# Optimization experiments

Hardware: AMD Instinct MI355X
Metric: run time of the kernel (lower is better)

## Reference

```python
import jax, jax.numpy as jnp
import numpy as np
import math

N_HEAD = 8
FACTOR = 1


def setup_inputs() -> dict:
    key = jax.random.key(0)
    kq, kk, kv = jax.random.split(key, 3)
    B, L, D = 16, 2048, 512
    return {
        "queries": jax.random.normal(kq, (B, L, D), dtype=jnp.float32),
        "keys": jax.random.normal(kk, (B, L, D), dtype=jnp.float32),
        "values": jax.random.normal(kv, (B, L, D), dtype=jnp.float32),
    }


def _autocorrelation(queries, keys, values):
    B, L, D = queries.shape
    H = N_HEAD
    E = D // H
    top_k = int(FACTOR * math.log(L))  # static: L is a Python int

    # (B,L,H,E) -> (B,H,E,L)
    q = queries.reshape(B, L, H, E).transpose(0, 2, 3, 1)
    k = keys.reshape(B, L, H, E).transpose(0, 2, 3, 1)
    v = values.reshape(B, L, H, E).transpose(0, 2, 3, 1)

    # period-based dependencies via FFT cross-correlation
    qf = jnp.fft.rfft(q, axis=-1)
    kf = jnp.fft.rfft(k, axis=-1)
    corr = jnp.fft.irfft(qf * jnp.conj(kf), n=L, axis=-1)  # (B,H,E,L)

    # time-delay aggregation (training path)
    mean_value = corr.mean(axis=(1, 2))                      # (B,L)
    index = jax.lax.top_k(mean_value.mean(axis=0), top_k)[1]  # (top_k,)
    weights = mean_value[:, index]                            # (B,top_k)
    tmp_corr = jax.nn.softmax(weights, axis=-1)               # (B,top_k)

    # roll values by each top-k delay and combine with softmax weights
    patterns = jax.vmap(lambda d: jnp.roll(v, -d, axis=-1))(index)  # (k,B,H,E,L)
    V = jnp.einsum('kbhel,bk->bhel', patterns, tmp_corr)            # (B,H,E,L)

    out = V.transpose(0, 3, 1, 2).reshape(B, L, D)
    corr_out = corr.transpose(0, 3, 1, 2).reshape(B, L, D)
    return out, corr_out


def reference(queries, keys, values):
    return _autocorrelation(queries, keys, values)
```

## Files before the change

kernel.cpp:

```cpp
#include <hip/hip_runtime.h>
#include <math.h>

#define B_  16
#define L_  2048
#define D_  512
#define K_  7
#define Q_  (B_*L_*D_)

__device__ __forceinline__ ushort f2bf(float x){
  uint u = __float_as_uint(x);
  u += 0x7FFFu + ((u >> 16) & 1u);
  return (ushort)(u >> 16);
}
__device__ __forceinline__ float bf2f(ushort h){
  return __uint_as_float((uint)h << 16);
}

__global__ __launch_bounds__(256) void kA(const float* __restrict__ q,
                                          const float* __restrict__ k,
                                          ushort* __restrict__ qT,
                                          ushort* __restrict__ kT) {
  __shared__ float t[64][65];
  const int l0 = blockIdx.x * 64, d0 = blockIdx.y * 64;
  const int b = blockIdx.z & 15, ten = blockIdx.z >> 4;
  const float*  __restrict__ src = ten ? k : q;
  ushort* __restrict__ dst = ten ? kT : qT;
  const int tid = threadIdx.x;
  const size_t ibase = (size_t)b * L_ * D_;
#pragma unroll
  for (int u = 0; u < 4; ++u) {
    const int idx = tid + (u << 8);
    const int row = idx >> 4;
    const int c   = (idx & 15) << 2;
    const float4 v = *(const float4*)&src[ibase + (size_t)(l0 + row) * D_ + d0 + c];
    t[row][c + 0] = v.x; t[row][c + 1] = v.y;
    t[row][c + 2] = v.z; t[row][c + 3] = v.w;
  }
  __syncthreads();
  const size_t obase = (size_t)b * D_ * L_;
#pragma unroll
  for (int u = 0; u < 4; ++u) {
    const int idx  = tid + (u << 8);
    const int drow = idx >> 4;
    const int c    = (idx & 15) << 2;
    ushort4 o;
    o.x = f2bf(t[c + 0][drow]); o.y = f2bf(t[c + 1][drow]);
    o.z = f2bf(t[c + 2][drow]); o.w = f2bf(t[c + 3][drow]);
    *(ushort4*)&dst[obase + (size_t)(d0 + drow) * L_ + l0 + c] = o;
  }
}

struct cf { float r, i; };
__device__ __forceinline__ cf cadd(cf a, cf b){ return {a.r+b.r, a.i+b.i}; }
__device__ __forceinline__ cf csub(cf a, cf b){ return {a.r-b.r, a.i-b.i}; }
__device__ __forceinline__ cf cmul(cf a, cf b){ return {a.r*b.r - a.i*b.i, a.r*b.i + a.i*b.r}; }
template<bool INV> __device__ __forceinline__ cf rot90(cf x){
  return INV ? cf{-x.i, x.r} : cf{x.i, -x.r};
}
__device__ __forceinline__ int swz(int a){ return a ^ (((a >> 4) ^ (a >> 8)) & 15); }
__device__ __forceinline__ cf ldx(const float2* __restrict__ p, int i){
  const float2 v = p[swz(i)]; return {v.x, v.y};
}
__device__ __forceinline__ void stx(float2* __restrict__ p, int i, cf v){
  p[swz(i)] = {v.r, v.i};
}

template<bool INV>
__device__ __forceinline__ void dft8(cf a[8], cf b[8]) {
  const float H = 0.70710678118654752440f;
  cf t0 = cadd(a[0],a[4]), t1 = cadd(a[1],a[5]), t2 = cadd(a[2],a[6]), t3 = cadd(a[3],a[7]);
  cf u0 = csub(a[0],a[4]), u1 = csub(a[1],a[5]), u2 = csub(a[2],a[6]), u3 = csub(a[3],a[7]);
  const cf w1 = INV ? cf{H,  H} : cf{ H, -H};
  const cf w3 = INV ? cf{-H, H} : cf{-H, -H};
  u1 = cmul(u1, w1);
  u2 = rot90<INV>(u2);
  u3 = cmul(u3, w3);
  { cf s0 = cadd(t0,t2), s1 = csub(t0,t2), s2 = cadd(t1,t3), s3 = rot90<INV>(csub(t1,t3));
    b[0]=cadd(s0,s2); b[4]=csub(s0,s2); b[2]=cadd(s1,s3); b[6]=csub(s1,s3); }
  { cf s0 = cadd(u0,u2), s1 = csub(u0,u2), s2 = cadd(u1,u3), s3 = rot90<INV>(csub(u1,u3));
    b[1]=cadd(s0,s2); b[5]=csub(s0,s2); b[3]=cadd(s1,s3); b[7]=csub(s1,s3); }
}

template<int LOG2S>
__device__ __forceinline__ void twiddle_store(cf b[8], float2* __restrict__ dst,
                                              int j, int p, float sgn_ang) {
  float sn, cs;
  __sincosf(sgn_ang * (float)(p << LOG2S), &sn, &cs);
  const cf w1{cs, sn};
  const cf w2 = cmul(w1, w1);
  const cf w3 = cmul(w2, w1);
  const cf w4 = cmul(w2, w2);
  const cf w5 = cmul(w3, w2);
  const cf w6 = cmul(w3, w3);
  const cf w7 = cmul(w4, w3);
  b[1] = cmul(b[1], w1); b[2] = cmul(b[2], w2); b[3] = cmul(b[3], w3);
  b[4] = cmul(b[4], w4); b[5] = cmul(b[5], w5); b[6] = cmul(b[6], w6);
  b[7] = cmul(b[7], w7);
  const int wb = j + 7 * (p << LOG2S);
#pragma unroll
  for (int k = 0; k < 8; ++k) stx(dst, wb + (k << LOG2S), b[k]);
}

#define ANG_ (-0.0030679615757712823f)

__device__ __forceinline__ void pass8_first(const ushort* __restrict__ qg,
                                            const ushort* __restrict__ kg,
                                            float2* __restrict__ dst, int j) {
  cf a[8], b[8];
#pragma unroll
  for (int l = 0; l < 8; ++l) {
    const int ix = j + (l << 8);
    a[l] = {bf2f(qg[ix]), bf2f(kg[ix])};
  }
  dft8<false>(a, b);
  twiddle_store<0>(b, dst, j, j, ANG_);
}

template<int LOG2S, bool INV>
__device__ __forceinline__ void pass8f2(const float2* __restrict__ src,
                                        float2* __restrict__ dst, int j) {
  const int p = j >> LOG2S;
  cf a[8], b[8];
#pragma unroll
  for (int l = 0; l < 8; ++l) a[l] = ldx(src, j + (l << 8));
  dft8<INV>(a, b);
  twiddle_store<LOG2S>(b, dst, j, p, INV ? -ANG_ : ANG_);
}

__device__ __forceinline__ void pass4_fwd(const float2* __restrict__ src,
                                          float2* __restrict__ dst, int j) {
#pragma unroll
  for (int h = 0; h < 2; ++h) {
    const int jj = j + (h << 8);
    cf a0 = ldx(src, jj), a1 = ldx(src, jj + 512), a2 = ldx(src, jj + 1024), a3 = ldx(src, jj + 1536);
    cf s0 = cadd(a0,a2), s1 = csub(a0,a2), s2 = cadd(a1,a3), s3 = rot90<false>(csub(a1,a3));
    stx(dst, jj,        cadd(s0,s2));
    stx(dst, jj + 512,  cadd(s1,s3));
    stx(dst, jj + 1024, csub(s0,s2));
    stx(dst, jj + 1536, csub(s1,s3));
  }
}

__device__ __forceinline__ void pass4_last(const float2* __restrict__ src,
                                           ushort* __restrict__ c0,
                                           ushort* __restrict__ c1, int j) {
  const float inv = 1.0f / (float)L_;
#pragma unroll
  for (int h = 0; h < 2; ++h) {
    const int jj = j + (h << 8);
    cf a0 = ldx(src, jj), a1 = ldx(src, jj + 512), a2 = ldx(src, jj + 1024), a3 = ldx(src, jj + 1536);
    cf s0 = cadd(a0,a2), s1 = csub(a0,a2), s2 = cadd(a1,a3), s3 = rot90<true>(csub(a1,a3));
    const cf o0 = cadd(s0,s2), o1 = cadd(s1,s3), o2 = csub(s0,s2), o3 = csub(s1,s3);
    c0[jj]        = f2bf(o0.r * inv);  c1[jj]        = f2bf(o0.i * inv);
    c0[jj + 512]  = f2bf(o1.r * inv);  c1[jj + 512]  = f2bf(o1.i * inv);
    c0[jj + 1024] = f2bf(o2.r * inv);  c1[jj + 1024] = f2bf(o2.i * inv);
    c0[jj + 1536] = f2bf(o3.r * inv);  c1[jj + 1536] = f2bf(o3.i * inv);
  }
}

__global__ __launch_bounds__(256) void kB(const ushort* __restrict__ qT,
                                          const ushort* __restrict__ kT,
                                          ushort* __restrict__ corrT) {
  __shared__ float2 A[L_];
  __shared__ float2 Bb[L_];
  const int tid = threadIdx.x;
  const size_t row0 = (size_t)(blockIdx.x * 2) * L_;
  const size_t row1 = row0 + L_;

  pass8_first(qT + row0, kT + row0, Bb, tid); __syncthreads();
  pass8f2<3, false>(Bb, A, tid);              __syncthreads();
  pass8f2<6, false>(A, Bb, tid);              __syncthreads();
  pass4_fwd(Bb, A, tid);                      __syncthreads();

  float s1r[4], s1i[4];
#pragma unroll
  for (int u = 0; u < 4; ++u) {
    const int f = tid + (u << 8);
    if (f == 0) {
      const cf z0 = ldx(A, 0), zn = ldx(A, 1024);
      s1r[u] = z0.r * z0.i;
      s1i[u] = zn.r * zn.i;
    } else {
      const cf a = ldx(A, f), am = ldx(A, 2048 - f);
      const float qr = 0.5f * (a.r + am.r), qi = 0.5f * (a.i - am.i);
      const float kr = 0.5f * (a.i + am.i), ki = 0.5f * (am.r - a.r);
      s1r[u] = qr * kr + qi * ki;
      s1i[u] = qi * kr - qr * ki;
    }
  }

  pass8_first(qT + row1, kT + row1, Bb, tid); __syncthreads();
  pass8f2<3, false>(Bb, A, tid);              __syncthreads();
  pass8f2<6, false>(A, Bb, tid);              __syncthreads();
  pass4_fwd(Bb, A, tid);                      __syncthreads();

#pragma unroll
  for (int u = 0; u < 4; ++u) {
    const int f = tid + (u << 8);
    if (f == 0) {
      const cf z0 = ldx(A, 0), zn = ldx(A, 1024);
      const float s2_0 = z0.r * z0.i, s2_n = zn.r * zn.i;
      stx(Bb, 0,    {s1r[0], s2_0});
      stx(Bb, 1024, {s1i[0], s2_n});
    } else {
      const cf a = ldx(A, f), am = ldx(A, 2048 - f);
      const float qr = 0.5f * (a.r + am.r), qi = 0.5f * (a.i - am.i);
      const float kr = 0.5f * (a.i + am.i), ki = 0.5f * (am.r - a.r);
      const float s2r = qr * kr + qi * ki, s2i = qi * kr - qr * ki;
      stx(Bb, f,        {s1r[u] - s2i,  s1i[u] + s2r});
      stx(Bb, 2048 - f, {s1r[u] + s2i, -s1i[u] + s2r});
    }
  }
  __syncthreads();

  pass8f2<0, true>(Bb, A, tid);               __syncthreads();
  pass8f2<3, true>(A, Bb, tid);               __syncthreads();
  pass8f2<6, true>(Bb, A, tid);               __syncthreads();
  pass4_last(A, corrT + row0, corrT + row1, tid);
}

__global__ __launch_bounds__(256) void kC(const ushort* __restrict__ corrT,
                                          float* __restrict__ corrOut,
                                          float* __restrict__ partial) {
  __shared__ float t[64][65];
  const int t0 = blockIdx.x * 64, d0 = blockIdx.y * 64, b = blockIdx.z;
  const int tid = threadIdx.x;
#pragma unroll
  for (int u = 0; u < 4; ++u) {
    const int idx  = tid + (u << 8);
    const int drow = idx >> 4;
    const int c    = (idx & 15) << 2;
    const ushort4 v = *(const ushort4*)&corrT[((size_t)b * D_ + d0 + drow) * L_ + t0 + c];
    t[drow][c + 0] = bf2f(v.x); t[drow][c + 1] = bf2f(v.y);
    t[drow][c + 2] = bf2f(v.z); t[drow][c + 3] = bf2f(v.w);
  }
  __syncthreads();
#pragma unroll
  for (int u = 0; u < 4; ++u) {
    const int idx  = tid + (u << 8);
    const int trow = idx >> 4;
    const int c    = (idx & 15) << 2;
    float4 o;
    o.x = t[c + 0][trow]; o.y = t[c + 1][trow];
    o.z = t[c + 2][trow]; o.w = t[c + 3][trow];
    *(float4*)&corrOut[((size_t)b * L_ + t0 + trow) * D_ + d0 + c] = o;
  }
  if (tid < 64) {
    float s = 0.f;
#pragma unroll
    for (int i = 0; i < 64; ++i) s += t[i][tid];
    partial[((size_t)b * 8 + blockIdx.y) * L_ + t0 + tid] = s;
  }
}

__global__ __launch_bounds__(256) void kD0(const float* __restrict__ partial,
                                           float* __restrict__ g) {
  __shared__ float red[4][64];
  const int tl = threadIdx.x & 63, rg = threadIdx.x >> 6;
  const int tau = blockIdx.x * 64 + tl;
  float s = 0.f;
  for (int i = rg; i < 128; i += 4) s += partial[(size_t)i * L_ + tau];
  red[rg][tl] = s;
  __syncthreads();
  if (rg == 0) g[tau] = red[0][tl] + red[1][tl] + red[2][tl] + red[3][tl];
}

__global__ __launch_bounds__(256) void kD1(const float* __restrict__ gin,
                                           const float* __restrict__ partial,
                                           int* __restrict__ oidx,
                                           float* __restrict__ ow) {
  __shared__ float g[L_];
  __shared__ float rv[256];
  __shared__ int   ri[256];
  __shared__ int   sidx[K_];
  const int tid = threadIdx.x;
#pragma unroll
  for (int u = 0; u < 8; ++u) g[tid + u * 256] = gin[tid + u * 256];
  __syncthreads();

  for (int it = 0; it < K_; ++it) {
    float bv = -1e30f; int bix = 1 << 30;
#pragma unroll
    for (int u = 0; u < 8; ++u) {
      const int tau = tid + u * 256;
      const float vv = g[tau];
      if (vv > bv || (vv == bv && tau < bix)) { bv = vv; bix = tau; }
    }
    rv[tid] = bv; ri[tid] = bix;
    __syncthreads();
    for (int off = 128; off > 0; off >>= 1) {
      if (tid < off) {
        const float v2 = rv[tid + off]; const int i2 = ri[tid + off];
        if (v2 > rv[tid] || (v2 == rv[tid] && i2 < ri[tid])) {
          rv[tid] = v2; ri[tid] = i2;
        }
      }
      __syncthreads();
    }
    if (tid == 0) { sidx[it] = ri[0]; g[ri[0]] = -3e38f; }
    __syncthreads();
  }

  if (tid < B_) {
    const int b = tid;
    float m[K_]; float mx = -1e30f;
    for (int kk = 0; kk < K_; ++kk) {
      float s = 0.f;
      for (int dt = 0; dt < 8; ++dt)
        s += partial[((size_t)b * 8 + dt) * L_ + sidx[kk]];
      m[kk] = s * (1.0f / 512.0f);
      mx = fmaxf(mx, m[kk]);
    }
    float sum = 0.f;
    for (int kk = 0; kk < K_; ++kk) { m[kk] = expf(m[kk] - mx); sum += m[kk]; }
    const float inv = 1.0f / sum;
    for (int kk = 0; kk < K_; ++kk) ow[b * K_ + kk] = m[kk] * inv;
  }
  if (tid < K_) oidx[tid] = sidx[tid];
}

__global__ __launch_bounds__(256) void kE(const float4* __restrict__ v4,
                                          const float* __restrict__ w,
                                          const int* __restrict__ idx,
                                          float4* __restrict__ out4) {
  const int bx = blockIdx.x;
  const int b  = bx >> 10;
  const int l  = ((bx & 1023) << 1) | (threadIdx.x >> 7);
  const int j  = threadIdx.x & 127;

  float ww[K_]; int rr[K_];
#pragma unroll
  for (int kk = 0; kk < K_; ++kk) {
    ww[kk] = w[b * K_ + kk];
    int r = l + idx[kk];
    if (r >= L_) r -= L_;
    rr[kk] = r;
  }
  const size_t vb = (size_t)b * L_ * 128;
  float4 acc = make_float4(0.f, 0.f, 0.f, 0.f);
#pragma unroll
  for (int kk = 0; kk < K_; ++kk) {
    const float4 vv = v4[vb + (size_t)rr[kk] * 128 + j];
    acc.x += ww[kk] * vv.x; acc.y += ww[kk] * vv.y;
    acc.z += ww[kk] * vv.z; acc.w += ww[kk] * vv.w;
  }
  out4[vb + (size_t)l * 128 + j] = acc;
}

extern "C" void kernel_launch(void* const* d_in, const int* in_sizes, int n_in,
                              void* d_out, int out_size, void* d_ws, size_t ws_size,
                              hipStream_t stream) {
  const float* q = (const float*)d_in[0];
  const float* k = (const float*)d_in[1];
  const float* v = (const float*)d_in[2];

  float* out     = (float*)d_out;
  float* corrOut = out + Q_;
  ushort* qT16 = (ushort*)out;
  ushort* kT16 = (ushort*)corrOut;

  ushort* corrT16 = (ushort*)d_ws;
  float*  partial = (float*)(corrT16 + Q_);
  float*  g2048   = partial + (size_t)B_ * 8 * L_;
  int*    oidx    = (int*)(g2048 + L_);
  float*  ow      = (float*)(oidx + 16);

  kA<<<dim3(L_ / 64, D_ / 64, B_ * 2), 256, 0, stream>>>(q, k, qT16, kT16);
  kB<<<(B_ * D_) / 2, 256, 0, stream>>>(qT16, kT16, corrT16);
  kC<<<dim3(L_ / 64, D_ / 64, B_), 256, 0, stream>>>(corrT16, corrOut, partial);
  kD0<<<32, 256, 0, stream>>>(partial, g2048);
  kD1<<<1, 256, 0, stream>>>(g2048, partial, oidx, ow);
  kE<<<(B_ * L_) / 2, 256, 0, stream>>>((const float4*)v, ow, oidx, (float4*)out);
}
```

Baseline: 187.2 us.

## Restructure 2048-point FFT from radix-8/8/8/4 into radix-16/16/8 passes

Replaces the four-pass shared-memory FFT (three radix-8 passes plus a radix-4 pass) with three passes: two radix-16 stages run by half the threads and a final radix-8 stage, for both forward and inverse transforms. This cuts the number of shared-memory round trips and barriers per transform. In exchange, half the block idles during the radix-16 stages, register pressure rises with 16-point butterflies, and the strided shared-memory store pattern may cause bank conflicts.

After: 210.2 us. +12.3%, slower.

```diff
diff --git a/kernel.cpp b/kernel.cpp
--- a/kernel.cpp
+++ b/kernel.cpp
@@ -81,80 +81,117 @@
     b[1]=cadd(s0,s2); b[5]=csub(s0,s2); b[3]=cadd(s1,s3); b[7]=csub(s1,s3); }
 }
 
-template<int LOG2S>
-__device__ __forceinline__ void twiddle_store(cf b[8], float2* __restrict__ dst,
-                                              int j, int p, float sgn_ang) {
-  float sn, cs;
-  __sincosf(sgn_ang * (float)(p << LOG2S), &sn, &cs);
+template<bool INV>
+__device__ __forceinline__ void dft16(cf a[16], cf o[16]) {
+  cf e_in[8], o_in[8], E[8], O[8];
+#pragma unroll
+  for (int i = 0; i < 8; ++i) { e_in[i] = a[2*i]; o_in[i] = a[2*i+1]; }
+  dft8<INV>(e_in, E);
+  dft8<INV>(o_in, O);
+  const float C1 = 0.92387953251128675613f, S1 = 0.38268343236508977173f;
+  const float H  = 0.70710678118654752440f;
+  const float sg = INV ? 1.0f : -1.0f;
+  const cf w1{ C1, sg*S1}, w2{ H, sg*H}, w3{ S1, sg*C1};
+  const cf w5{-S1, sg*C1}, w6{-H, sg*H}, w7{-C1, sg*S1};
+  cf t;
+  t = O[0];             o[0]=cadd(E[0],t); o[8] =csub(E[0],t);
+  t = cmul(O[1], w1);   o[1]=cadd(E[1],t); o[9] =csub(E[1],t);
+  t = cmul(O[2], w2);   o[2]=cadd(E[2],t); o[10]=csub(E[2],t);
+  t = cmul(O[3], w3);   o[3]=cadd(E[3],t); o[11]=csub(E[3],t);
+  t = rot90<INV>(O[4]); o[4]=cadd(E[4],t); o[12]=csub(E[4],t);
+  t = cmul(O[5], w5);   o[5]=cadd(E[5],t); o[13]=csub(E[5],t);
+  t = cmul(O[6], w6);   o[6]=cadd(E[6],t); o[14]=csub(E[6],t);
+  t = cmul(O[7], w7);   o[7]=cadd(E[7],t); o[15]=csub(E[7],t);
+}
+
+#define ANG_ (-0.0030679615757712823f)
+
+__device__ __forceinline__ void twiddle16(cf b[16], float ang) {
+  float sn, cs; __sincosf(ang, &sn, &cs);
   const cf w1{cs, sn};
-  const cf w2 = cmul(w1, w1);
-  const cf w3 = cmul(w2, w1);
-  const cf w4 = cmul(w2, w2);
-  const cf w5 = cmul(w3, w2);
-  const cf w6 = cmul(w3, w3);
-  const cf w7 = cmul(w4, w3);
-  b[1] = cmul(b[1], w1); b[2] = cmul(b[2], w2); b[3] = cmul(b[3], w3);
-  b[4] = cmul(b[4], w4); b[5] = cmul(b[5], w5); b[6] = cmul(b[6], w6);
-  b[7] = cmul(b[7], w7);
-  const int wb = j + 7 * (p << LOG2S);
-#pragma unroll
-  for (int k = 0; k < 8; ++k) stx(dst, wb + (k << LOG2S), b[k]);
-}
-
-#define ANG_ (-0.0030679615757712823f)
-
-__device__ __forceinline__ void pass8_first(const ushort* __restrict__ qg,
-                                            const ushort* __restrict__ kg,
-                                            float2* __restrict__ dst, int j) {
+  const cf w2 = cmul(w1,w1);
+  const cf w3 = cmul(w2,w1);
+  const cf w4 = cmul(w2,w2);
+  const cf w5 = cmul(w3,w2);
+  const cf w6 = cmul(w3,w3);
+  const cf w7 = cmul(w4,w3);
+  const cf w8 = cmul(w4,w4);
+  const cf w9 = cmul(w5,w4);
+  const cf w10= cmul(w5,w5);
+  const cf w11= cmul(w6,w5);
+  const cf w12= cmul(w6,w6);
+  const cf w13= cmul(w7,w6);
+  const cf w14= cmul(w7,w7);
+  const cf w15= cmul(w8,w7);
+  b[1]=cmul(b[1],w1);  b[2]=cmul(b[2],w2);  b[3]=cmul(b[3],w3);
+  b[4]=cmul(b[4],w4);  b[5]=cmul(b[5],w5);  b[6]=cmul(b[6],w6);
+  b[7]=cmul(b[7],w7);  b[8]=cmul(b[8],w8);  b[9]=cmul(b[9],w9);
+  b[10]=cmul(b[10],w10); b[11]=cmul(b[11],w11); b[12]=cmul(b[12],w12);
+  b[13]=cmul(b[13],w13); b[14]=cmul(b[14],w14); b[15]=cmul(b[15],w15);
+}
+
+__device__ __forceinline__ void p16_first(const ushort* __restrict__ qg,
+                                          const ushort* __restrict__ kg,
+                                          float2* __restrict__ dst, int j) {
+  cf a[16], b[16];
+#pragma unroll
+  for (int l = 0; l < 16; ++l) {
+    const int ix = j + (l << 7);
+    a[l] = {bf2f(qg[ix]), bf2f(kg[ix])};
+  }
+  dft16<false>(a, b);
+  twiddle16(b, ANG_ * (float)j);
+#pragma unroll
+  for (int k = 0; k < 16; ++k) stx(dst, (j << 4) + k, b[k]);
+}
+
+__device__ __forceinline__ void p16_s1_inv(const float2* __restrict__ src,
+                                           float2* __restrict__ dst, int j) {
+  cf a[16], b[16];
+#pragma unroll
+  for (int l = 0; l < 16; ++l) a[l] = ldx(src, j + (l << 7));
+  dft16<true>(a, b);
+  twiddle16(b, -ANG_ * (float)j);
+#pragma unroll
+  for (int k = 0; k < 16; ++k) stx(dst, (j << 4) + k, b[k]);
+}
+
+template<bool INV>
+__device__ __forceinline__ void p16_mid(const float2* __restrict__ src,
+                                        float2* __restrict__ dst, int j) {
+  const int p = j >> 4, q = j & 15;
+  cf a[16], b[16];
+#pragma unroll
+  for (int l = 0; l < 16; ++l) a[l] = ldx(src, j + (l << 7));
+  dft16<INV>(a, b);
+  twiddle16(b, (INV ? -ANG_ : ANG_) * (float)(p << 4));
+  const int base = q + (p << 8);
+#pragma unroll
+  for (int k = 0; k < 16; ++k) stx(dst, base + (k << 4), b[k]);
+}
+
+__device__ __forceinline__ void p8_final(const float2* __restrict__ src,
+                                         float2* __restrict__ dst, int j) {
   cf a[8], b[8];
 #pragma unroll
-  for (int l = 0; l < 8; ++l) {
-    const int ix = j + (l << 8);
-    a[l] = {bf2f(qg[ix]), bf2f(kg[ix])};
-  }
+  for (int l = 0; l < 8; ++l) a[l] = ldx(src, j + (l << 8));
   dft8<false>(a, b);
-  twiddle_store<0>(b, dst, j, j, ANG_);
-}
-
-template<int LOG2S, bool INV>
-__device__ __forceinline__ void pass8f2(const float2* __restrict__ src,
-                                        float2* __restrict__ dst, int j) {
-  const int p = j >> LOG2S;
+#pragma unroll
+  for (int k = 0; k < 8; ++k) stx(dst, j + (k << 8), b[k]);
+}
+
+__device__ __forceinline__ void p8_final_store(const float2* __restrict__ src,
+                                               ushort* __restrict__ c0,
+                                               ushort* __restrict__ c1, int j) {
   cf a[8], b[8];
 #pragma unroll
   for (int l = 0; l < 8; ++l) a[l] = ldx(src, j + (l << 8));
-  dft8<INV>(a, b);
-  twiddle_store<LOG2S>(b, dst, j, p, INV ? -ANG_ : ANG_);
-}
-
-__device__ __forceinline__ void pass4_fwd(const float2* __restrict__ src,
-                                          float2* __restrict__ dst, int j) {
-#pragma unroll
-  for (int h = 0; h < 2; ++h) {
-    const int jj = j + (h << 8);
-    cf a0 = ldx(src, jj), a1 = ldx(src, jj + 512), a2 = ldx(src, jj + 1024), a3 = ldx(src, jj + 1536);
-    cf s0 = cadd(a0,a2), s1 = csub(a0,a2), s2 = cadd(a1,a3), s3 = rot90<false>(csub(a1,a3));
-    stx(dst, jj,        cadd(s0,s2));
-    stx(dst, jj + 512,  cadd(s1,s3));
-    stx(dst, jj + 1024, csub(s0,s2));
-    stx(dst, jj + 1536, csub(s1,s3));
-  }
-}
-
-__device__ __forceinline__ void pass4_last(const float2* __restrict__ src,
-                                           ushort* __restrict__ c0,
-                                           ushort* __restrict__ c1, int j) {
+  dft8<true>(a, b);
   const float inv = 1.0f / (float)L_;
 #pragma unroll
-  for (int h = 0; h < 2; ++h) {
-    const int jj = j + (h << 8);
-    cf a0 = ldx(src, jj), a1 = ldx(src, jj + 512), a2 = ldx(src, jj + 1024), a3 = ldx(src, jj + 1536);
-    cf s0 = cadd(a0,a2), s1 = csub(a0,a2), s2 = cadd(a1,a3), s3 = rot90<true>(csub(a1,a3));
-    const cf o0 = cadd(s0,s2), o1 = cadd(s1,s3), o2 = csub(s0,s2), o3 = csub(s1,s3);
-    c0[jj]        = f2bf(o0.r * inv);  c1[jj]        = f2bf(o0.i * inv);
-    c0[jj + 512]  = f2bf(o1.r * inv);  c1[jj + 512]  = f2bf(o1.i * inv);
-    c0[jj + 1024] = f2bf(o2.r * inv);  c1[jj + 1024] = f2bf(o2.i * inv);
-    c0[jj + 1536] = f2bf(o3.r * inv);  c1[jj + 1536] = f2bf(o3.i * inv);
+  for (int k = 0; k < 8; ++k) {
+    c0[j + (k << 8)] = f2bf(b[k].r * inv);
+    c1[j + (k << 8)] = f2bf(b[k].i * inv);
   }
 }
 
@@ -164,13 +201,13 @@
   __shared__ float2 A[L_];
   __shared__ float2 Bb[L_];
   const int tid = threadIdx.x;
+  const bool lo = tid < 128;
   const size_t row0 = (size_t)(blockIdx.x * 2) * L_;
   const size_t row1 = row0 + L_;
 
-  pass8_first(qT + row0, kT + row0, Bb, tid); __syncthreads();
-  pass8f2<3, false>(Bb, A, tid);              __syncthreads();
-  pass8f2<6, false>(A, Bb, tid);              __syncthreads();
-  pass4_fwd(Bb, A, tid);                      __syncthreads();
+  if (lo) p16_first(qT + row0, kT + row0, A, tid);  __syncthreads();
+  if (lo) p16_mid<false>(A, Bb, tid);               __syncthreads();
+  p8_final(Bb, A, tid);                             __syncthreads();
 
   float s1r[4], s1i[4];
 #pragma unroll
@@ -188,11 +225,11 @@
       s1i[u] = qi * kr - qr * ki;
     }
   }
-
-  pass8_first(qT + row1, kT + row1, Bb, tid); __syncthreads();
-  pass8f2<3, false>(Bb, A, tid);              __syncthreads();
-  pass8f2<6, false>(A, Bb, tid);              __syncthreads();
-  pass4_fwd(Bb, A, tid);                      __syncthreads();
+  __syncthreads();
+
+  if (lo) p16_first(qT + row1, kT + row1, A, tid);  __syncthreads();
+  if (lo) p16_mid<false>(A, Bb, tid);               __syncthreads();
+  p8_final(Bb, A, tid);                             __syncthreads();
 
 #pragma unroll
   for (int u = 0; u < 4; ++u) {
@@ -213,10 +250,9 @@
   }
   __syncthreads();
 
-  pass8f2<0, true>(Bb, A, tid);               __syncthreads();
-  pass8f2<3, true>(A, Bb, tid);               __syncthreads();
-  pass8f2<6, true>(Bb, A, tid);               __syncthreads();
-  pass4_last(A, corrT + row0, corrT + row1, tid);
+  if (lo) p16_s1_inv(Bb, A, tid);                   __syncthreads();
+  if (lo) p16_mid<true>(A, Bb, tid);                __syncthreads();
+  p8_final_store(Bb, corrT + row0, corrT + row1, tid);
 }
 
 __global__ __launch_bounds__(256) void kC(const ushort* __restrict__ corrT,
```
